# Kernel optimization log

Measured on AMD Instinct MI355X. Metric: run time of the kernel, lower is better.

The kernel has to match this reference:

```python
import jax, jax.numpy as jnp
import numpy as np

B, C, H, W = 8, 256, 128, 128
INTER = 64      # in_channels // 4
C8 = INTER // 8 # query/key channels


def setup_inputs() -> dict:
    key = jax.random.key(0)
    ks = jax.random.split(key, 12)
    f = lambda k, shp, s=0.05: (jax.random.normal(k, shp, jnp.float32) * s)
    return dict(
        x_exmplar=f(ks[0], (B, C, H, W), 1.0),
        x_query=f(ks[1], (B, C, H, W), 1.0),
        conv_ex_w=f(ks[2], (INTER, C, 3, 3)),
        bn_ex_s=jnp.ones((INTER,), jnp.float32), bn_ex_b=jnp.zeros((INTER,), jnp.float32),
        conv_q_w=f(ks[3], (INTER, C, 3, 3)),
        bn_q_s=jnp.ones((INTER,), jnp.float32), bn_q_b=jnp.zeros((INTER,), jnp.float32),
        q_w=f(ks[4], (C8, INTER)), q_b=jnp.zeros((C8,), jnp.float32),
        k_w=f(ks[5], (C8, INTER)), k_b=jnp.zeros((C8,), jnp.float32),
        v_w=f(ks[6], (INTER, INTER)), v_b=jnp.zeros((INTER,), jnp.float32),
        gamma_1=jnp.float32(0.1), gamma_2=jnp.float32(0.1),
        tail_ex_w=f(ks[7], (C, INTER, 3, 3)),
        bn_tex_s=jnp.ones((C,), jnp.float32), bn_tex_b=jnp.zeros((C,), jnp.float32),
        tail_q_w=f(ks[8], (C, INTER, 3, 3)),
        bn_tq_s=jnp.ones((C,), jnp.float32), bn_tq_b=jnp.zeros((C,), jnp.float32),
    )


def _conv_bn_relu(x, w, s, b):
    # 3x3 conv (pad 1, no bias) + eval-mode BatchNorm (running mean 0 / var 1 at init) + ReLU
    y = jax.lax.conv_general_dilated(x, w, (1, 1), ((1, 1), (1, 1)),
                                     dimension_numbers=('NCHW', 'OIHW', 'NCHW'))
    return jax.nn.relu(y * s[None, :, None, None] + b[None, :, None, None])


def _rattention(xe, xq, qw, qb, kw, kb, vw, vb, g1, g2):
    b_, c_, h_, w_ = xq.shape
    q = jnp.einsum('oc,bchw->bohw', qw, xq) + qb[None, :, None, None]  # [B,C8,H,W]
    k = jnp.einsum('oc,bchw->bohw', kw, xe) + kb[None, :, None, None]
    v = jnp.einsum('oc,bchw->bohw', vw, xe) + vb[None, :, None, None]  # [B,INTER,H,W]
    # column (H-axis) energies, diagonal (self) masked with -inf
    eH = jnp.einsum('bciw,bcjw->biwj', q, k)                    # [B,H,W,H]
    diag = jnp.eye(h_, dtype=bool)[None, :, None, :]            # (1,H,1,H) over (i,j)
    eH = jnp.where(diag, -jnp.inf, eH)
    # row (W-axis) energies (no mask, matches original)
    eW = jnp.einsum('bchi,bchj->bhij', q, k)                    # [B,H,W,W]
    att = jax.nn.softmax(jnp.concatenate([eH, eW], axis=-1), axis=-1)
    attH, attW = att[..., :h_], att[..., h_:]
    outH = jnp.einsum('bcjw,bhwj->bchw', v, attH)
    outW = jnp.einsum('bchj,bhwj->bchw', v, attW)
    # LR diagonal branch; softmax over trailing singleton dim == ones (kept for fidelity)
    qd = jnp.diagonal(q, axis1=2, axis2=3)                      # [B,C8,H]
    kd = jnp.diagonal(k, axis1=2, axis2=3).transpose(0, 2, 1)   # [B,H,C8]
    vd = jnp.diagonal(v, axis1=2, axis2=3)                      # [B,INTER,H]
    eLR = jnp.einsum('bhc,bcj->bhj', kd, qd)                    # [B,H,H]
    outLR = jax.nn.softmax(jnp.einsum('bch,bhj->bcj', vd, eLR)[..., None], axis=3)  # [B,INTER,H,1]
    # RL branch: diagonal of the transposed map == same main diagonal -> identical to LR
    outRL = outLR
    s = outH + outW + outLR + outRL   # broadcast (B,INTER,H,1) over W
    return g1 * s + xe, g2 * s + xq


def reference(x_exmplar, x_query, conv_ex_w, bn_ex_s, bn_ex_b, conv_q_w, bn_q_s, bn_q_b,
              q_w, q_b, k_w, k_b, v_w, v_b, gamma_1, gamma_2,
              tail_ex_w, bn_tex_s, bn_tex_b, tail_q_w, bn_tq_s, bn_tq_b):
    xe = _conv_bn_relu(x_exmplar, conv_ex_w, bn_ex_s, bn_ex_b)
    xq = _conv_bn_relu(x_query, conv_q_w, bn_q_s, bn_q_b)
    for _ in range(2):  # recurrence=2
        xe, xq = _rattention(xe, xq, q_w, q_b, k_w, k_b, v_w, v_b, gamma_1, gamma_2)
    xe = _conv_bn_relu(xe, tail_ex_w, bn_tex_s, bn_tex_b)
    xq = _conv_bn_relu(xq, tail_q_w, bn_tq_s, bn_tq_b)
    return xe, xq
```

## Files before the change

### kernel.cpp

```cpp
#include <hip/hip_runtime.h>

constexpr int BB = 8;
constexpr int CC = 256;
constexpr int HH = 128;
constexpr int WW = 128;
constexpr int INTER = 64;
constexpr size_t NPIX = (size_t)HH * WW;
constexpr size_t C64SZ = (size_t)BB * INTER * NPIX;
constexpr size_t QSZ   = (size_t)BB * 8 * NPIX;
constexpr size_t STATSZ = (size_t)BB * HH * WW;
constexpr size_t OUTHALF = (size_t)BB * CC * NPIX;
constexpr size_t WT_ELEMS = (size_t)9 * 64 * 256;

typedef __attribute__((ext_vector_type(8))) __bf16 bf16x8;
typedef __attribute__((ext_vector_type(4))) float f32x4;
typedef __attribute__((ext_vector_type(4))) short short4v;

__device__ inline short f2bf(float f) {
    union { float f; unsigned u; } a; a.f = f;
    unsigned r = a.u + 0x7fffu + ((a.u >> 16) & 1u);
    return (short)(r >> 16);
}

__global__ __launch_bounds__(256) void wprep_kernel(
    const float* __restrict__ wgt, short* __restrict__ wt, int OC, int IC)
{
    int idx = blockIdx.x * 256 + threadIdx.x;
    int n = 9 * OC * IC;
    if (idx >= n) return;
    int ic = idx & (IC - 1);
    int t  = idx / IC;
    int oc = t & (OC - 1);
    int pos = t / OC;
    wt[idx] = f2bf(wgt[((size_t)oc * IC + ic) * 9 + pos]);
}

template<int IC, int OC, int R, int NT, int BLK, int MINW>
__global__ __launch_bounds__(BLK, MINW) void conv_mfma(
    const float* __restrict__ x, const short* __restrict__ wt,
    const float* __restrict__ bns, const float* __restrict__ bnb,
    float* __restrict__ out)
{
    constexpr int ROWS = R + 2;
    constexpr int NCH  = IC / 32;
    constexpr int NPIXT = R * 128;
    constexpr int NWN  = NPIXT / (NT * 16);
    constexpr int TOTAL_UNITS = ROWS * 8 * 32;
    constexpr int NU   = TOTAL_UNITS / BLK;

    __shared__ __align__(16) short xs[ROWS * 130 * 40];

    const int tid = threadIdx.x;
    const int b   = blockIdx.x;
    const int h0  = blockIdx.y * R;
    const int l   = tid & 63;
    const int ln  = l & 15;
    const int q   = l >> 4;
    const int wv  = tid >> 6;
    const int nbase = (wv % NWN) * (NT * 16);
    const int oc0w  = (wv / NWN) * 64;

    f32x4 acc[4][NT];
#pragma unroll
    for (int mt = 0; mt < 4; ++mt)
#pragma unroll
        for (int nt = 0; nt < NT; ++nt)
            acc[mt][nt] = (f32x4){0.f, 0.f, 0.f, 0.f};

    const float* xb = x + (size_t)b * IC * NPIX;

    f32x4 pf[NU][4];

    if (tid < ROWS * 16) {
        int row  = tid >> 4;
        int colh = (tid & 8) ? 129 : 0;
        int icg  = tid & 7;
        short4v z; z.x = 0; z.y = 0; z.z = 0; z.w = 0;
        *(short4v*)&xs[(row * 130 + colh) * 40 + icg * 4] = z;
    }

    auto issue = [&](int ch) {
        const int ic0 = ch * 32;
#pragma unroll
        for (int i = 0; i < NU; ++i) {
            int u    = i * BLK + tid;
            int row  = u >> 8;
            int icq  = (u >> 5) & 7;
            int colq = u & 31;
            int grow = h0 - 1 + row;
            if ((unsigned)grow < 128u) {
                const float* p = xb + ((size_t)(ic0 + icq * 4) * 128 + grow) * 128 + colq * 4;
#pragma unroll
                for (int j = 0; j < 4; ++j)
                    pf[i][j] = *(const f32x4*)(p + (size_t)j * NPIX);
            } else {
#pragma unroll
                for (int j = 0; j < 4; ++j)
                    pf[i][j] = (f32x4){0.f, 0.f, 0.f, 0.f};
            }
        }
    };

    auto commit = [&]() {
#pragma unroll
        for (int i = 0; i < NU; ++i) {
            int u    = i * BLK + tid;
            int row  = u >> 8;
            int icq  = (u >> 5) & 7;
            int colq = u & 31;
#pragma unroll
            for (int k = 0; k < 4; ++k) {
                short4v pk;
                pk.x = f2bf(pf[i][0][k]);
                pk.y = f2bf(pf[i][1][k]);
                pk.z = f2bf(pf[i][2][k]);
                pk.w = f2bf(pf[i][3][k]);
                *(short4v*)&xs[(row * 130 + colq * 4 + k + 1) * 40 + icq * 4] = pk;
            }
        }
    };

    issue(0);
    commit();
    __syncthreads();

    for (int ch = 0; ch < NCH; ++ch) {
        if (ch + 1 < NCH) issue(ch + 1);

        const int ic0 = ch * 32;
        for (int dh = 0; dh < 3; ++dh) {
#pragma unroll
            for (int dw = 0; dw < 3; ++dw) {
                const int pos = dh * 3 + dw;
                bf16x8 a[4];
#pragma unroll
                for (int mt = 0; mt < 4; ++mt)
                    a[mt] = *(const bf16x8*)(wt +
                        (size_t)(pos * OC + oc0w + mt * 16 + ln) * IC + ic0 + q * 8);
#pragma unroll
                for (int nt = 0; nt < NT; ++nt) {
                    int pix  = nbase + nt * 16 + ln;
                    int rowi = (pix >> 7) + dh;
                    int wpos = (pix & 127) + dw;
                    bf16x8 bfr = *(const bf16x8*)&xs[(rowi * 130 + wpos) * 40 + q * 8];
#pragma unroll
                    for (int mt = 0; mt < 4; ++mt)
                        acc[mt][nt] = __builtin_amdgcn_mfma_f32_16x16x32_bf16(
                            a[mt], bfr, acc[mt][nt], 0, 0, 0);
                }
            }
        }
        __syncthreads();
        if (ch + 1 < NCH) {
            commit();
            __syncthreads();
        }
    }

#pragma unroll
    for (int mt = 0; mt < 4; ++mt) {
#pragma unroll
        for (int r = 0; r < 4; ++r) {
            int oc = oc0w + mt * 16 + q * 4 + r;
            float s   = bns[oc];
            float bb2 = bnb[oc];
#pragma unroll
            for (int nt = 0; nt < NT; ++nt) {
                int pix = nbase + nt * 16 + ln;
                int h = h0 + (pix >> 7), w = pix & 127;
                float v = fmaxf(acc[mt][nt][r] * s + bb2, 0.f);
                out[(((size_t)b * OC + oc) * 128 + h) * 128 + w] = v;
            }
        }
    }
}

__global__ __launch_bounds__(256) void qk_kernel(
    const float* __restrict__ xq, const float* __restrict__ xe,
    const float* __restrict__ qw, const float* __restrict__ qb,
    const float* __restrict__ kw, const float* __restrict__ kb,
    float* __restrict__ q, float* __restrict__ k)
{
    size_t p = (size_t)blockIdx.x * 256 + threadIdx.x;
    int b = (int)(p >> 14);
    int pix = (int)(p & 16383);
    const float* xqb = xq + (size_t)b * 64 * NPIX + pix;
    const float* xeb = xe + (size_t)b * 64 * NPIX + pix;
    float qa[8], ka[8];
#pragma unroll
    for (int o = 0; o < 8; ++o) { qa[o] = qb[o]; ka[o] = kb[o]; }
    for (int c = 0; c < 64; ++c) {
        float xv = xqb[(size_t)c * NPIX];
        float ev = xeb[(size_t)c * NPIX];
#pragma unroll
        for (int o = 0; o < 8; ++o) {
            qa[o] += qw[o * 64 + c] * xv;
            ka[o] += kw[o * 64 + c] * ev;
        }
    }
#pragma unroll
    for (int o = 0; o < 8; ++o) {
        q[((size_t)b * 8 + o) * NPIX + pix] = qa[o];
        k[((size_t)b * 8 + o) * NPIX + pix] = ka[o];
    }
}

__global__ __launch_bounds__(256) void v_kernel(
    const float* __restrict__ xe,
    const float* __restrict__ vw, const float* __restrict__ vb,
    float* __restrict__ v)
{
    size_t p = (size_t)blockIdx.x * 256 + threadIdx.x;
    int b = (int)(p >> 14);
    int pix = (int)(p & 16383);
    int oc0 = blockIdx.y * 32;
    const float* xeb = xe + (size_t)b * 64 * NPIX + pix;
    float acc[32];
#pragma unroll
    for (int o = 0; o < 32; ++o) acc[o] = vb[oc0 + o];
    for (int c = 0; c < 64; ++c) {
        float ev = xeb[(size_t)c * NPIX];
#pragma unroll
        for (int o = 0; o < 32; ++o) acc[o] += vw[(oc0 + o) * 64 + c] * ev;
    }
#pragma unroll
    for (int o = 0; o < 32; ++o)
        v[((size_t)b * 64 + oc0 + o) * NPIX + pix] = acc[o];
}

__global__ __launch_bounds__(256) void attn_col_kernel(
    const float* __restrict__ q, const float* __restrict__ k,
    const float* __restrict__ v,
    float* __restrict__ outT, float* __restrict__ mC, float* __restrict__ sC)
{
    __shared__ float qs[8][128];
    __shared__ float ks[8][128];
    __shared__ float vs[64][129];
    __shared__ float E[32][129];

    const int tid = threadIdx.x;
    const int w = blockIdx.x;
    const int b = blockIdx.y;

    for (int i = tid; i < 1024; i += 256) {
        int c = i >> 7, h = i & 127;
        qs[c][h] = q[(((size_t)b * 8 + c) * 128 + h) * 128 + w];
        ks[c][h] = k[(((size_t)b * 8 + c) * 128 + h) * 128 + w];
    }
    for (int i = tid; i < 8192; i += 256) {
        int c = i >> 7, j = i & 127;
        vs[c][j] = v[(((size_t)b * 64 + c) * 128 + j) * 128 + w];
    }
    __syncthreads();

    const int jj = tid & 127;
    const int hi = tid >> 7;

    for (int hc = 0; hc < 4; ++hc) {
        const int h0 = hc * 32;
#pragma unroll
        for (int e = 0; e < 16; ++e) {
            int i = e * 2 + hi;
            float a = 0.f;
#pragma unroll
            for (int c = 0; c < 8; ++c) a += qs[c][h0 + i] * ks[c][jj];
            if (h0 + i == jj) a = -1e30f;
            E[i][jj] = a;
        }
        __syncthreads();
        {
            int row = tid >> 3, l8 = tid & 7;
            float m = -1e30f;
#pragma unroll
            for (int t = 0; t < 16; ++t) m = fmaxf(m, E[row][l8 + t * 8]);
            m = fmaxf(m, __shfl_xor(m, 1));
            m = fmaxf(m, __shfl_xor(m, 2));
            m = fmaxf(m, __shfl_xor(m, 4));
            float s = 0.f;
#pragma unroll
            for (int t = 0; t < 16; ++t) {
                int j = l8 + t * 8;
                float pp = __expf(E[row][j] - m);
                E[row][j] = pp;
                s += pp;
            }
            s += __shfl_xor(s, 1);
            s += __shfl_xor(s, 2);
            s += __shfl_xor(s, 4);
            if (l8 == 0) {
                mC[((size_t)b * 128 + (h0 + row)) * 128 + w] = m;
                sC[((size_t)b * 128 + (h0 + row)) * 128 + w] = s;
            }
        }
        __syncthreads();
        {
            int c0 = (tid & 15) * 4;
            int i0 = (tid >> 4) * 2;
            float acc[4][2];
#pragma unroll
            for (int a = 0; a < 4; ++a) { acc[a][0] = 0.f; acc[a][1] = 0.f; }
            for (int j = 0; j < 128; ++j) {
                float p0 = E[i0][j], p1 = E[i0 + 1][j];
#pragma unroll
                for (int a = 0; a < 4; ++a) {
                    float vv = vs[c0 + a][j];
                    acc[a][0] += vv * p0;
                    acc[a][1] += vv * p1;
                }
            }
#pragma unroll
            for (int a = 0; a < 4; ++a) {
                size_t base = (((size_t)b * 128 + w) * 64 + (c0 + a)) * 128 + h0 + i0;
                outT[base]     = acc[a][0];
                outT[base + 1] = acc[a][1];
            }
        }
        __syncthreads();
    }
}

__global__ __launch_bounds__(256) void attn_row_kernel(
    const float* __restrict__ q, const float* __restrict__ k,
    const float* __restrict__ v,
    float* __restrict__ outS, float* __restrict__ mR, float* __restrict__ sR)
{
    __shared__ float qs[8][128];
    __shared__ float ks[8][128];
    __shared__ float vs[64][129];
    __shared__ float E[32][129];

    const int tid = threadIdx.x;
    const int h = blockIdx.x;
    const int b = blockIdx.y;

    for (int i = tid; i < 1024; i += 256) {
        int c = i >> 7, x = i & 127;
        qs[c][x] = q[(((size_t)b * 8 + c) * 128 + h) * 128 + x];
        ks[c][x] = k[(((size_t)b * 8 + c) * 128 + h) * 128 + x];
    }
    for (int i = tid; i < 8192; i += 256) {
        int c = i >> 7, j = i & 127;
        vs[c][j] = v[(((size_t)b * 64 + c) * 128 + h) * 128 + j];
    }
    __syncthreads();

    const int jj = tid & 127;
    const int hi = tid >> 7;

    for (int wc = 0; wc < 4; ++wc) {
        const int w0 = wc * 32;
#pragma unroll
        for (int e = 0; e < 16; ++e) {
            int i = e * 2 + hi;
            float a = 0.f;
#pragma unroll
            for (int c = 0; c < 8; ++c) a += qs[c][w0 + i] * ks[c][jj];
            E[i][jj] = a;
        }
        __syncthreads();
        {
            int row = tid >> 3, l8 = tid & 7;
            float m = -1e30f;
#pragma unroll
            for (int t = 0; t < 16; ++t) m = fmaxf(m, E[row][l8 + t * 8]);
            m = fmaxf(m, __shfl_xor(m, 1));
            m = fmaxf(m, __shfl_xor(m, 2));
            m = fmaxf(m, __shfl_xor(m, 4));
            float s = 0.f;
#pragma unroll
            for (int t = 0; t < 16; ++t) {
                int j = l8 + t * 8;
                float pp = __expf(E[row][j] - m);
                E[row][j] = pp;
                s += pp;
            }
            s += __shfl_xor(s, 1);
            s += __shfl_xor(s, 2);
            s += __shfl_xor(s, 4);
            if (l8 == 0) {
                mR[((size_t)b * 128 + h) * 128 + (w0 + row)] = m;
                sR[((size_t)b * 128 + h) * 128 + (w0 + row)] = s;
            }
        }
        __syncthreads();
        {
            int c0 = (tid & 15) * 4;
            int i0 = (tid >> 4) * 2;
            float acc[4][2];
#pragma unroll
            for (int a = 0; a < 4; ++a) { acc[a][0] = 0.f; acc[a][1] = 0.f; }
            for (int j = 0; j < 128; ++j) {
                float p0 = E[i0][j], p1 = E[i0 + 1][j];
#pragma unroll
                for (int a = 0; a < 4; ++a) {
                    float vv = vs[c0 + a][j];
                    acc[a][0] += vv * p0;
                    acc[a][1] += vv * p1;
                }
            }
#pragma unroll
            for (int a = 0; a < 4; ++a) {
                size_t base = (((size_t)b * 64 + (c0 + a)) * 128 + h) * 128 + w0 + i0;
                outS[base]     = acc[a][0];
                outS[base + 1] = acc[a][1];
            }
        }
        __syncthreads();
    }
}

__global__ __launch_bounds__(256) void merge_kernel(
    const float* __restrict__ T1, const float* __restrict__ S2,
    const float* __restrict__ mC, const float* __restrict__ sC,
    const float* __restrict__ mR, const float* __restrict__ sR,
    const float* __restrict__ g1p, const float* __restrict__ g2p,
    float* __restrict__ xe, float* __restrict__ xq)
{
    __shared__ float mc[128], sc[128], mr[128], sr[128];
    const int tid = threadIdx.x;
    const int h = blockIdx.x;
    const int b = blockIdx.y;
    if (tid < 128) {
        size_t o = ((size_t)b * 128 + h) * 128 + tid;
        mc[tid] = mC[o]; sc[tid] = sC[o];
        mr[tid] = mR[o]; sr[tid] = sR[o];
    }
    float g1 = g1p[0], g2 = g2p[0];
    __syncthreads();
    for (int i = tid; i < 8192; i += 256) {
        int c = i >> 7, w = i & 127;
        float oc_ = T1[(((size_t)b * 128 + w) * 64 + c) * 128 + h];
        float ow_ = S2[(((size_t)b * 64 + c) * 128 + h) * 128 + w];
        float m  = fmaxf(mc[w], mr[w]);
        float ec = __expf(mc[w] - m);
        float er = __expf(mr[w] - m);
        float denom = sc[w] * ec + sr[w] * er;
        float sval = (oc_ * ec + ow_ * er) / denom + 2.0f;
        size_t p = (((size_t)b * 64 + c) * 128 + h) * 128 + w;
        xe[p] += g1 * sval;
        xq[p] += g2 * sval;
    }
}

extern "C" void kernel_launch(void* const* d_in, const int* in_sizes, int n_in,
                              void* d_out, int out_size, void* d_ws, size_t ws_size,
                              hipStream_t stream)
{
    const float* x_ex = (const float*)d_in[0];
    const float* x_q  = (const float*)d_in[1];
    const float* cew  = (const float*)d_in[2];
    const float* bes  = (const float*)d_in[3];
    const float* beb  = (const float*)d_in[4];
    const float* cqw  = (const float*)d_in[5];
    const float* bqs  = (const float*)d_in[6];
    const float* bqb  = (const float*)d_in[7];
    const float* qw   = (const float*)d_in[8];
    const float* qb   = (const float*)d_in[9];
    const float* kw   = (const float*)d_in[10];
    const float* kb   = (const float*)d_in[11];
    const float* vw   = (const float*)d_in[12];
    const float* vb   = (const float*)d_in[13];
    const float* g1   = (const float*)d_in[14];
    const float* g2   = (const float*)d_in[15];
    const float* tew  = (const float*)d_in[16];
    const float* bts  = (const float*)d_in[17];
    const float* btb  = (const float*)d_in[18];
    const float* tqw  = (const float*)d_in[19];
    const float* btqs = (const float*)d_in[20];
    const float* btqb = (const float*)d_in[21];

    float* out = (float*)d_out;

    short* wt0 = (short*)d_ws;
    short* wt1 = wt0 + WT_ELEMS;
    short* wt2 = wt1 + WT_ELEMS;
    short* wt3 = wt2 + WT_ELEMS;
    float* Wf  = (float*)(wt3 + WT_ELEMS);
    float* xe = Wf;
    float* xq = Wf + C64SZ;
    float* v  = Wf + 2 * C64SZ;
    float* q  = Wf + 3 * C64SZ;
    float* k  = q + QSZ;

    float* T1 = out;
    float* S2 = out + C64SZ;
    float* mC = out + 2 * C64SZ;
    float* sC = mC + STATSZ;
    float* mR = sC + STATSZ;
    float* sR = mR + STATSZ;

    wprep_kernel<<<576, 256, 0, stream>>>(cew, wt0, 64, 256);
    wprep_kernel<<<576, 256, 0, stream>>>(cqw, wt1, 64, 256);
    wprep_kernel<<<576, 256, 0, stream>>>(tew, wt2, 256, 64);
    wprep_kernel<<<576, 256, 0, stream>>>(tqw, wt3, 256, 64);

    conv_mfma<256, 64, 2, 2, 512, 4><<<dim3(8, 64), 512, 0, stream>>>(x_ex, wt0, bes, beb, xe);
    conv_mfma<256, 64, 2, 2, 512, 4><<<dim3(8, 64), 512, 0, stream>>>(x_q,  wt1, bqs, bqb, xq);

    for (int round = 0; round < 2; ++round) {
        qk_kernel<<<512, 256, 0, stream>>>(xq, xe, qw, qb, kw, kb, q, k);
        v_kernel<<<dim3(512, 2), 256, 0, stream>>>(xe, vw, vb, v);
        attn_col_kernel<<<dim3(128, 8), 256, 0, stream>>>(q, k, v, T1, mC, sC);
        attn_row_kernel<<<dim3(128, 8), 256, 0, stream>>>(q, k, v, S2, mR, sR);
        merge_kernel<<<dim3(128, 8), 256, 0, stream>>>(T1, S2, mC, sC, mR, sR, g1, g2, xe, xq);
    }

    conv_mfma<64, 256, 1, 8, 256, 2><<<dim3(8, 128), 256, 0, stream>>>(xe, wt2, bts, btb, out);
    conv_mfma<64, 256, 1, 8, 256, 2><<<dim3(8, 128), 256, 0, stream>>>(xq, wt3, btqs, btqb, out + OUTHALF);
}
```

Measured before the change: 1.597 ms.

## Pre-convert conv inputs to bf16 channel-blocked layout and stage weights in LDS

Adds a conversion kernel that turns fp32 NCHW activations into bf16 in a [B][IC/32][H][W][32] layout. The conv kernel can then load 16-byte vectors directly instead of converting while it stages tiles. Conv weights for each 32-channel chunk are now staged into a swizzled LDS buffer rather than read from global memory per MFMA. The tail convs are also split over output-channel blocks via a third grid dimension. Costs are extra conversion passes, extra global memory traffic for the bf16 copies, and more LDS per block, which may lower occupancy.

```diff
diff --git a/kernel.cpp b/kernel.cpp
--- a/kernel.cpp
+++ b/kernel.cpp
@@ -15,6 +15,7 @@
 typedef __attribute__((ext_vector_type(8))) __bf16 bf16x8;
 typedef __attribute__((ext_vector_type(4))) float f32x4;
 typedef __attribute__((ext_vector_type(4))) short short4v;
+typedef __attribute__((ext_vector_type(8))) short short8v;
 
 __device__ inline short f2bf(float f) {
     union { float f; unsigned u; } a; a.f = f;
@@ -35,9 +36,45 @@
     wt[idx] = f2bf(wgt[((size_t)oc * IC + ic) * 9 + pos]);
 }
 
+template<int G>
+__global__ __launch_bounds__(256) void cvt_kernel(
+    const float* __restrict__ x, short* __restrict__ o)
+{
+    __shared__ float ts[32][133];
+    const int tid = threadIdx.x;
+    const int h = blockIdx.x;
+    const int g = blockIdx.y % G;
+    const int b = blockIdx.y / G;
+
+    {
+        int c  = tid >> 3;
+        int w0 = (tid & 7) * 16;
+        const float* src = x + ((size_t)(b * (G * 32) + g * 32 + c)) * NPIX + (size_t)h * 128 + w0;
+#pragma unroll
+        for (int j = 0; j < 4; ++j) {
+            f32x4 vv = *(const f32x4*)(src + j * 4);
+#pragma unroll
+            for (int e = 0; e < 4; ++e) ts[c][w0 + j * 4 + e] = vv[e];
+        }
+    }
+    __syncthreads();
+
+#pragma unroll
+    for (int it = 0; it < 2; ++it) {
+        int u  = it * 256 + tid;
+        int c8 = u & 3;
+        int w  = u >> 2;
+        short8v pk;
+#pragma unroll
+        for (int j = 0; j < 8; ++j) pk[j] = f2bf(ts[c8 * 8 + j][w]);
+        *(short8v*)(o + (((size_t)(b * G + g) * 128 + h) * 128 + w) * 32 + c8 * 8) = pk;
+    }
+}
+
 template<int IC, int OC, int R, int NT, int BLK, int MINW>
 __global__ __launch_bounds__(BLK, MINW) void conv_mfma(
-    const float* __restrict__ x, const short* __restrict__ wt,
+    const short* __restrict__ xb,
+    const short* __restrict__ wt,
     const float* __restrict__ bns, const float* __restrict__ bnb,
     float* __restrict__ out)
 {
@@ -45,20 +82,24 @@
     constexpr int NCH  = IC / 32;
     constexpr int NPIXT = R * 128;
     constexpr int NWN  = NPIXT / (NT * 16);
-    constexpr int TOTAL_UNITS = ROWS * 8 * 32;
-    constexpr int NU   = TOTAL_UNITS / BLK;
+    constexpr int XSU  = ROWS * 512;
+    constexpr int NU   = XSU / BLK;
+    constexpr int WSU  = 9 * 64 * 4;
+    constexpr int WIT  = (WSU + BLK - 1) / BLK;
 
     __shared__ __align__(16) short xs[ROWS * 130 * 40];
+    __shared__ __align__(16) short ws[9 * 64 * 32];
 
     const int tid = threadIdx.x;
     const int b   = blockIdx.x;
     const int h0  = blockIdx.y * R;
+    const int oc0b = blockIdx.z * 64;
     const int l   = tid & 63;
     const int ln  = l & 15;
     const int q   = l >> 4;
     const int wv  = tid >> 6;
     const int nbase = (wv % NWN) * (NT * 16);
-    const int oc0w  = (wv / NWN) * 64;
+    const int aoff  = (q ^ ((ln >> 1) & 3)) * 8;
 
     f32x4 acc[4][NT];
 #pragma unroll
@@ -67,36 +108,30 @@
         for (int nt = 0; nt < NT; ++nt)
             acc[mt][nt] = (f32x4){0.f, 0.f, 0.f, 0.f};
 
-    const float* xb = x + (size_t)b * IC * NPIX;
-
-    f32x4 pf[NU][4];
-
-    if (tid < ROWS * 16) {
-        int row  = tid >> 4;
-        int colh = (tid & 8) ? 129 : 0;
-        int icg  = tid & 7;
-        short4v z; z.x = 0; z.y = 0; z.z = 0; z.w = 0;
-        *(short4v*)&xs[(row * 130 + colh) * 40 + icg * 4] = z;
-    }
+    if (tid < ROWS * 8) {
+        int row = tid >> 3;
+        int rem = tid & 7;
+        int colh = (rem >> 2) ? 129 : 0;
+        int quad = rem & 3;
+        short8v z = (short8v){0,0,0,0,0,0,0,0};
+        *(short8v*)&xs[(row * 130 + colh) * 40 + quad * 8] = z;
+    }
+
+    short8v pf[NU];
 
     auto issue = [&](int ch) {
-        const int ic0 = ch * 32;
 #pragma unroll
         for (int i = 0; i < NU; ++i) {
             int u    = i * BLK + tid;
-            int row  = u >> 8;
-            int icq  = (u >> 5) & 7;
-            int colq = u & 31;
+            int quad = u & 3;
+            int col  = (u >> 2) & 127;
+            int row  = u >> 9;
             int grow = h0 - 1 + row;
             if ((unsigned)grow < 128u) {
-                const float* p = xb + ((size_t)(ic0 + icq * 4) * 128 + grow) * 128 + colq * 4;
-#pragma unroll
-                for (int j = 0; j < 4; ++j)
-                    pf[i][j] = *(const f32x4*)(p + (size_t)j * NPIX);
+                pf[i] = *(const short8v*)(xb +
+                    (((size_t)(b * NCH + ch) * 128 + grow) * 128 + col) * 32 + quad * 8);
             } else {
-#pragma unroll
-                for (int j = 0; j < 4; ++j)
-                    pf[i][j] = (f32x4){0.f, 0.f, 0.f, 0.f};
+                pf[i] = (short8v){0,0,0,0,0,0,0,0};
             }
         }
     };
@@ -105,29 +140,38 @@
 #pragma unroll
         for (int i = 0; i < NU; ++i) {
             int u    = i * BLK + tid;
-            int row  = u >> 8;
-            int icq  = (u >> 5) & 7;
-            int colq = u & 31;
-#pragma unroll
-            for (int k = 0; k < 4; ++k) {
-                short4v pk;
-                pk.x = f2bf(pf[i][0][k]);
-                pk.y = f2bf(pf[i][1][k]);
-                pk.z = f2bf(pf[i][2][k]);
-                pk.w = f2bf(pf[i][3][k]);
-                *(short4v*)&xs[(row * 130 + colq * 4 + k + 1) * 40 + icq * 4] = pk;
+            int quad = u & 3;
+            int col  = (u >> 2) & 127;
+            int row  = u >> 9;
+            *(short8v*)&xs[(row * 130 + col + 1) * 40 + quad * 8] = pf[i];
+        }
+    };
+
+    auto stage_ws = [&](int ch) {
+#pragma unroll
+        for (int it = 0; it < WIT; ++it) {
+            int u = it * BLK + tid;
+            if (u < WSU) {
+                int quad = u & 3;
+                int oc   = (u >> 2) & 63;
+                int pos  = u >> 8;
+                short8v wv8 = *(const short8v*)(wt +
+                    (size_t)(pos * OC + oc0b + oc) * IC + ch * 32 + quad * 8);
+                int row  = pos * 64 + oc;
+                int slot = quad ^ ((row >> 1) & 3);
+                *(short8v*)&ws[row * 32 + slot * 8] = wv8;
             }
         }
     };
 
     issue(0);
     commit();
+    stage_ws(0);
     __syncthreads();
 
     for (int ch = 0; ch < NCH; ++ch) {
         if (ch + 1 < NCH) issue(ch + 1);
 
-        const int ic0 = ch * 32;
         for (int dh = 0; dh < 3; ++dh) {
 #pragma unroll
             for (int dw = 0; dw < 3; ++dw) {
@@ -135,8 +179,7 @@
                 bf16x8 a[4];
 #pragma unroll
                 for (int mt = 0; mt < 4; ++mt)
-                    a[mt] = *(const bf16x8*)(wt +
-                        (size_t)(pos * OC + oc0w + mt * 16 + ln) * IC + ic0 + q * 8);
+                    a[mt] = *(const bf16x8*)&ws[(pos * 64 + mt * 16 + ln) * 32 + aoff];
 #pragma unroll
                 for (int nt = 0; nt < NT; ++nt) {
                     int pix  = nbase + nt * 16 + ln;
@@ -153,6 +196,7 @@
         __syncthreads();
         if (ch + 1 < NCH) {
             commit();
+            stage_ws(ch + 1);
             __syncthreads();
         }
     }
@@ -161,7 +205,7 @@
     for (int mt = 0; mt < 4; ++mt) {
 #pragma unroll
         for (int r = 0; r < 4; ++r) {
-            int oc = oc0w + mt * 16 + q * 4 + r;
+            int oc = oc0b + mt * 16 + q * 4 + r;
             float s   = bns[oc];
             float bb2 = bnb[oc];
 #pragma unroll
@@ -481,7 +525,11 @@
     float* v  = Wf + 2 * C64SZ;
     float* q  = Wf + 3 * C64SZ;
     float* k  = q + QSZ;
-
+    short* xeb16 = (short*)(k + QSZ);
+    short* xqb16 = xeb16 + C64SZ;
+
+    short* xb16e = (short*)out;
+    short* xb16q = xb16e + (size_t)BB * CC * NPIX;
     float* T1 = out;
     float* S2 = out + C64SZ;
     float* mC = out + 2 * C64SZ;
@@ -494,8 +542,11 @@
     wprep_kernel<<<576, 256, 0, stream>>>(tew, wt2, 256, 64);
     wprep_kernel<<<576, 256, 0, stream>>>(tqw, wt3, 256, 64);
 
-    conv_mfma<256, 64, 2, 2, 512, 4><<<dim3(8, 64), 512, 0, stream>>>(x_ex, wt0, bes, beb, xe);
-    conv_mfma<256, 64, 2, 2, 512, 4><<<dim3(8, 64), 512, 0, stream>>>(x_q,  wt1, bqs, bqb, xq);
+    cvt_kernel<8><<<dim3(128, 64), 256, 0, stream>>>(x_ex, xb16e);
+    cvt_kernel<8><<<dim3(128, 64), 256, 0, stream>>>(x_q,  xb16q);
+
+    conv_mfma<256, 64, 2, 2, 512, 4><<<dim3(8, 64, 1), 512, 0, stream>>>(xb16e, wt0, bes, beb, xe);
+    conv_mfma<256, 64, 2, 2, 512, 4><<<dim3(8, 64, 1), 512, 0, stream>>>(xb16q, wt1, bqs, bqb, xq);
 
     for (int round = 0; round < 2; ++round) {
         qk_kernel<<<512, 256, 0, stream>>>(xq, xe, qw, qb, kw, kb, q, k);
@@ -505,6 +556,9 @@
         merge_kernel<<<dim3(128, 8), 256, 0, stream>>>(T1, S2, mC, sC, mR, sR, g1, g2, xe, xq);
     }
 
-    conv_mfma<64, 256, 1, 8, 256, 2><<<dim3(8, 128), 256, 0, stream>>>(xe, wt2, bts, btb, out);
-    conv_mfma<64, 256, 1, 8, 256, 2><<<dim3(8, 128), 256, 0, stream>>>(xq, wt3, btqs, btqb, out + OUTHALF);
-}
+    cvt_kernel<2><<<dim3(128, 16), 256, 0, stream>>>(xe, xeb16);
+    cvt_kernel<2><<<dim3(128, 16), 256, 0, stream>>>(xq, xqb16);
+
+    conv_mfma<64, 256, 1, 2, 256, 2><<<dim3(8, 128, 4), 256, 0, stream>>>(xeb16, wt2, bts, btb, out);
+    conv_mfma<64, 256, 1, 2, 256, 2><<<dim3(8, 128, 4), 256, 0, stream>>>(xqb16, wt3, btqs, btqb, out + OUTHALF);
+}
```

Result: faster. 1.398 ms (-12.5%).
